# Performance work log

Hardware: AMD Instinct MI355X
Metric: run time of the kernel (lower is better)

Reference implementation:

```python
import jax, jax.numpy as jnp
import numpy as np

B, S, NU, ML, H, V = 32, 256, 4, 9, 768, 30522


def setup_inputs() -> dict:
    key = jax.random.key(0)
    ks = jax.random.split(key, 13)
    s = 1.0 / np.sqrt(H)
    return {
        "x": jax.random.randint(ks[0], (B, S), 0, V),
        "decoder_input": jax.random.normal(ks[1], (B, NU, H), jnp.float32) * 0.02,
        "encoder_output": jax.random.normal(ks[2], (B, S, H), jnp.float32) * 0.02,
        "hidden": jax.random.normal(ks[3], (1, B, H), jnp.float32) * 0.02,
        "max_len": ML,
        "teacher": jax.random.randint(ks[4], (B, NU, ML), 0, V),
        "embed_w": jax.random.normal(ks[5], (V, H), jnp.float32) * 0.02,
        "gru_w_ih": jax.random.uniform(ks[6], (3 * H, H), jnp.float32, -s, s),
        "gru_w_hh": jax.random.uniform(ks[7], (3 * H, H), jnp.float32, -s, s),
        "gru_b_ih": jax.random.uniform(ks[8], (3 * H,), jnp.float32, -s, s),
        "gru_b_hh": jax.random.uniform(ks[9], (3 * H,), jnp.float32, -s, s),
        "w_gen_w": jax.random.uniform(ks[10], (1, 3 * H), jnp.float32, -s, s),
        "w_gen_b": jax.random.uniform(ks[11], (1,), jnp.float32, -s, s),
    }


def reference(x, decoder_input, encoder_output, hidden, max_len, teacher,
              embed_w, gru_w_ih, gru_w_hh, gru_b_ih, gru_b_hh, w_gen_w, w_gen_b):
    pad_mask = (x == 0)                       # [B, S]
    b, nu, h_dim = decoder_input.shape
    h0 = hidden[0]                            # [B, H]

    # Teacher-forced input sequence for every (update, step): [NU*ML, B, H]
    tf = embed_w[teacher[:, :, :max_len - 1]]           # [B, NU, ML-1, H]
    tf = jnp.moveaxis(tf, 0, 2)                          # [NU, ML-1, B, H]
    first = jnp.swapaxes(decoder_input, 0, 1)[:, None]   # [NU, 1, B, H]
    ws = jnp.concatenate([first, tf], axis=1).reshape(nu * max_len, b, h_dim)

    def gru_cell(w, h):
        gi = w @ gru_w_ih.T + gru_b_ih        # [B, 3H]
        gh = h @ gru_w_hh.T + gru_b_hh
        i_r, i_z, i_n = jnp.split(gi, 3, axis=-1)
        h_r, h_z, h_n = jnp.split(gh, 3, axis=-1)
        r = jax.nn.sigmoid(i_r + h_r)
        z = jax.nn.sigmoid(i_z + h_z)
        n = jnp.tanh(i_n + r * h_n)
        return (1.0 - z) * n + z * h

    batch_idx = jnp.arange(b)[:, None]

    def step(h, w):
        h = gru_cell(w, h)                                    # [B, H]
        attn_e = jnp.einsum('bsh,bh->bs', encoder_output, h)  # [B, S]
        attn_e = jnp.where(pad_mask, -1e9, attn_e)
        attn_history = jax.nn.softmax(attn_e, axis=-1)        # [B, S]
        attn_vocab = jax.nn.softmax(h @ embed_w.T, axis=-1)   # [B, V]
        context = jnp.einsum('bs,bsh->bh', attn_history, encoder_output)
        gate_in = jnp.concatenate([w, h, context], axis=-1)   # [B, 3H]
        p_gen = jax.nn.sigmoid(gate_in @ w_gen_w.T + w_gen_b) # [B, 1]
        p_ctx = jnp.zeros_like(attn_vocab).at[batch_idx, x].add(attn_history)
        p_final = p_gen * attn_vocab + (1.0 - p_gen) * p_ctx  # [B, V]
        return h, p_final

    _, outs = jax.lax.scan(step, h0, ws)          # [NU*ML, B, V]
    outs = outs.reshape(nu, max_len, b, -1)       # [NU, ML, B, V]
    return jnp.transpose(outs, (2, 0, 1, 3))      # [B, NU, ML, V]
```

## Files before the change

kernel.cpp:

```cpp
#include <hip/hip_runtime.h>
#include <math.h>

#define BB_ 32
#define SS_ 256
#define HH_ 768
#define VV_ 30522
#define TT_ 36
#define MM_ 1152
#define NBLK_GRU 48

#define CE0 5860224
#define CE1 7433088
#define CE2 7875456
#define CE3 8317824
#define CE4 8323968

typedef __bf16 bf16x8 __attribute__((ext_vector_type(8)));
typedef __bf16 bf16x4 __attribute__((ext_vector_type(4)));
typedef float f32x4 __attribute__((ext_vector_type(4)));
typedef float f32x2 __attribute__((ext_vector_type(2)));
typedef unsigned int u32x4 __attribute__((ext_vector_type(4)));

__device__ __forceinline__ float sigmoidf_(float x) { return 1.f / (1.f + expf(-x)); }

__device__ __forceinline__ void async_load16(const void* g, void* l) {
  __builtin_amdgcn_global_load_lds(
      (const __attribute__((address_space(1))) void*)g,
      (__attribute__((address_space(3))) void*)l, 16, 0, 0);
}

__global__ __launch_bounds__(256) void cvt_all(const float* __restrict__ s0,
                                               const float* __restrict__ s1,
                                               const float* __restrict__ s2,
                                               const float* __restrict__ s3,
                                               const float* __restrict__ s4,
                                               __bf16* __restrict__ d0,
                                               __bf16* __restrict__ d1,
                                               __bf16* __restrict__ d2,
                                               __bf16* __restrict__ d3,
                                               __bf16* __restrict__ d4) {
  int i = blockIdx.x * 256 + threadIdx.x;
  const float* s; __bf16* d; int off;
  if (i < CE0)      { s = s0; d = d0; off = 0; }
  else if (i < CE1) { s = s1; d = d1; off = CE0; }
  else if (i < CE2) { s = s2; d = d2; off = CE1; }
  else if (i < CE3) { s = s3; d = d3; off = CE2; }
  else if (i < CE4) { s = s4; d = d4; off = CE3; }
  else return;
  int j = i - off;
  float4 v = reinterpret_cast<const float4*>(s)[j];
  bf16x4 o;
  o[0] = (__bf16)v.x; o[1] = (__bf16)v.y; o[2] = (__bf16)v.z; o[3] = (__bf16)v.w;
  reinterpret_cast<bf16x4*>(d)[j] = o;
}

__global__ __launch_bounds__(256) void build_ws(const float* __restrict__ dec,
                                                const int* __restrict__ teacher,
                                                const float* __restrict__ embed,
                                                __bf16* __restrict__ wsbf) {
  int idx = blockIdx.x * 256 + threadIdx.x;
  if (idx >= MM_ * HH_) return;
  int m = idx / HH_, k = idx - m * HH_;
  int tau = m >> 5, b = m & 31;
  int u = tau / 9, tt = tau - u * 9;
  float v;
  if (tt == 0) v = dec[((size_t)b * 4 + u) * HH_ + k];
  else v = embed[(size_t)teacher[(b * 4 + u) * 9 + tt - 1] * HH_ + k];
  wsbf[idx] = (__bf16)v;
}

__global__ __launch_bounds__(256) void enc_gate(const float* __restrict__ enc,
                                                const float* __restrict__ wgen,
                                                float* __restrict__ encg) {
  int row = blockIdx.x * 4 + (threadIdx.x >> 6);
  int lane = threadIdx.x & 63;
  const float* er = enc + (size_t)row * HH_;
  float ssum = 0.f;
#pragma unroll
  for (int i = 0; i < 12; ++i) ssum += er[i * 64 + lane] * wgen[1536 + i * 64 + lane];
  for (int off = 32; off; off >>= 1) ssum += __shfl_down(ssum, off);
  if (lane == 0) encg[row] = ssum;
}

template <int MODE>
__global__ __launch_bounds__(256) void gemm_bt2(const __bf16* __restrict__ A,
                                                const __bf16* __restrict__ Bm,
                                                float* __restrict__ C,
                                                float* __restrict__ rowsum,
                                                int Nreal, int ldC) {
  __shared__ __bf16 As[128 * 32];
  __shared__ __bf16 Bs[128 * 32];
  const int tid = threadIdx.x;
  const int lane = tid & 63, wave = tid >> 6;
  const int wm = wave >> 1, wn = wave & 1;
  const int q = lane >> 4, ln = lane & 15;
  const int m0 = blockIdx.y * 128, n0 = blockIdx.x * 128;
  const int srow = (wave << 5) + (lane >> 2);
  const int kc = lane & 3;
  const size_t aoff = (size_t)(m0 + srow) * HH_ + kc * 8;
  const size_t aoff2 = aoff + 16 * HH_;
  int br1 = n0 + srow;      if (br1 >= Nreal) br1 = Nreal - 1;
  int br2 = n0 + srow + 16; if (br2 >= Nreal) br2 = Nreal - 1;
  __bf16* lA1 = &As[srow * 32 + kc * 8];
  __bf16* lA2 = &As[(srow + 16) * 32 + kc * 8];
  __bf16* lB1 = &Bs[srow * 32 + kc * 8];
  __bf16* lB2 = &Bs[(srow + 16) * 32 + kc * 8];
  f32x4 acc[4][4] = {};
  for (int kb = 0; kb < 24; ++kb) {
    const int k0 = kb << 5;
    async_load16(A + aoff + k0, lA1);
    async_load16(A + aoff2 + k0, lA2);
    async_load16(Bm + (size_t)br1 * HH_ + kc * 8 + k0, lB1);
    async_load16(Bm + (size_t)br2 * HH_ + kc * 8 + k0, lB2);
    __syncthreads();
    bf16x8 af[4], bfr[4];
#pragma unroll
    for (int mi = 0; mi < 4; ++mi)
      af[mi] = *reinterpret_cast<const bf16x8*>(&As[(wm * 64 + mi * 16 + ln) * 32 + q * 8]);
#pragma unroll
    for (int ni = 0; ni < 4; ++ni)
      bfr[ni] = *reinterpret_cast<const bf16x8*>(&Bs[(wn * 64 + ni * 16 + ln) * 32 + q * 8]);
#pragma unroll
    for (int mi = 0; mi < 4; ++mi)
#pragma unroll
      for (int ni = 0; ni < 4; ++ni)
        acc[mi][ni] = __builtin_amdgcn_mfma_f32_16x16x32_bf16(af[mi], bfr[ni], acc[mi][ni], 0, 0, 0);
    __syncthreads();
  }
#pragma unroll
  for (int mi = 0; mi < 4; ++mi)
#pragma unroll
    for (int r2 = 0; r2 < 4; ++r2) {
      const int m = m0 + wm * 64 + mi * 16 + q * 4 + r2;
      if (MODE == 0) {
#pragma unroll
        for (int ni = 0; ni < 4; ++ni) {
          int n = n0 + wn * 64 + ni * 16 + ln;
          if (n < Nreal) C[(size_t)m * ldC + n] = acc[mi][ni][r2];
        }
      } else {
        float part = 0.f;
#pragma unroll
        for (int ni = 0; ni < 4; ++ni) {
          int n = n0 + wn * 64 + ni * 16 + ln;
          float e = expf(fminf(acc[mi][ni][r2], 60.f));
          if (n < Nreal) {
            __builtin_nontemporal_store(e, &C[(size_t)m * ldC + n]);
            part += e;
          }
        }
#pragma unroll
        for (int o = 1; o < 16; o <<= 1) part += __shfl_xor(part, o);
        if (ln == 0) atomicAdd(rowsum + m, part);
      }
    }
}

__global__ __launch_bounds__(128, 1) void gru_scan(const __bf16* __restrict__ hid_bf,
                                                   const float* __restrict__ H0,
                                                   const __bf16* __restrict__ Whh,
                                                   const float* __restrict__ GI,
                                                   const float* __restrict__ bih,
                                                   const float* __restrict__ bhh,
                                                   __bf16* __restrict__ Ah,
                                                   __bf16* __restrict__ Hx,
                                                   unsigned* __restrict__ flags) {
  __shared__ __bf16 WhhS[48 * HH_];
  const int tid = threadIdx.x, lane = tid & 63;
  const int mi = tid >> 6;
  const int q = lane >> 4, ln = lane & 15;
  const int jH = blockIdx.x * 16 + ln;
  for (int i = tid; i < 48 * 96; i += 128) {
    int row = i / 96, cs = i - row * 96;
    int g = row >> 4, jl = row & 15;
    bf16x8 v = *reinterpret_cast<const bf16x8*>(
        &Whh[((size_t)(g * 768 + blockIdx.x * 16 + jl)) * HH_ + cs * 8]);
    *reinterpret_cast<bf16x8*>(&WhhS[row * HH_ + ((cs ^ (row & 7)) * 8)]) = v;
  }
  const float bir = bih[jH], biz = bih[jH + 768], bin_ = bih[jH + 1536];
  const float bhr = bhh[jH], bhz = bhh[jH + 768], bhn = bhh[jH + 1536];
  float hc[4];
#pragma unroll
  for (int r2 = 0; r2 < 4; ++r2)
    hc[r2] = H0[(size_t)(mi * 16 + q * 4 + r2) * HH_ + jH];
  const __bf16* w0 = &WhhS[(0 + ln) * HH_];
  const __bf16* w1 = &WhhS[(16 + ln) * HH_];
  const __bf16* w2 = &WhhS[(32 + ln) * HH_];
  const int swz = (ln & 7) * 8;
  float gir[4], giz[4], gin[4];
#pragma unroll
  for (int r2 = 0; r2 < 4; ++r2) {
    const float* gi = GI + (size_t)(mi * 16 + q * 4 + r2) * 2304;
    gir[r2] = gi[jH]; giz[r2] = gi[jH + 768]; gin[r2] = gi[jH + 1536];
  }
  __syncthreads();
  for (int tau = 0; tau < TT_; ++tau) {
    const __bf16* arow = tau ? (Hx + (size_t)(((tau - 1) & 1) * 32 + mi * 16 + ln) * HH_)
                             : (hid_bf + (size_t)(mi * 16 + ln) * HH_);
    u32x4 raw[24];
#pragma unroll
    for (int kb = 0; kb < 24; ++kb) {
      const __bf16* ap = arow + kb * 32 + q * 8;
      asm volatile("global_load_dwordx4 %0, %1, off sc1"
                   : "=v"(raw[kb]) : "v"(ap) : "memory");
    }
    asm volatile("s_waitcnt vmcnt(0)" ::: "memory");
    __builtin_amdgcn_sched_barrier(0);
    f32x4 a0 = {}, a1 = {}, a2 = {};
#pragma unroll
    for (int kb = 0; kb < 24; ++kb) {
      bf16x8 a = __builtin_bit_cast(bf16x8, raw[kb]);
      int kl = (kb * 32 + q * 8) ^ swz;
      bf16x8 b0 = *reinterpret_cast<const bf16x8*>(w0 + kl);
      bf16x8 b1 = *reinterpret_cast<const bf16x8*>(w1 + kl);
      bf16x8 b2 = *reinterpret_cast<const bf16x8*>(w2 + kl);
      a0 = __builtin_amdgcn_mfma_f32_16x16x32_bf16(a, b0, a0, 0, 0, 0);
      a1 = __builtin_amdgcn_mfma_f32_16x16x32_bf16(a, b1, a1, 0, 0, 0);
      a2 = __builtin_amdgcn_mfma_f32_16x16x32_bf16(a, b2, a2, 0, 0, 0);
    }
    __bf16* hxc = Hx + (size_t)((tau & 1) * 32) * HH_;
#pragma unroll
    for (int r2 = 0; r2 < 4; ++r2) {
      int b = mi * 16 + q * 4 + r2;
      float r = sigmoidf_(gir[r2] + bir + a0[r2] + bhr);
      float z = sigmoidf_(giz[r2] + biz + a1[r2] + bhz);
      float n = tanhf(gin[r2] + bin_ + r * (a2[r2] + bhn));
      float h = (1.f - z) * n + z * hc[r2];
      hc[r2] = h;
      float hp = __shfl_xor(h, 1);
      __bf16 hb = (__bf16)h, hpb = (__bf16)hp;
      unsigned lo = (unsigned)__builtin_bit_cast(unsigned short, hb);
      unsigned hi = (unsigned)__builtin_bit_cast(unsigned short, hpb);
      if (!(ln & 1)) {
        unsigned u = lo | (hi << 16);
        *reinterpret_cast<unsigned*>(&Ah[((size_t)b * TT_ + tau) * HH_ + jH]) = u;
        if (tau < TT_ - 1)
          __hip_atomic_store(reinterpret_cast<unsigned*>(&hxc[(size_t)b * HH_ + jH]), u,
                             __ATOMIC_RELAXED, __HIP_MEMORY_SCOPE_AGENT);
      }
    }
    if (tau < TT_ - 1) {
      asm volatile("s_waitcnt vmcnt(0)" ::: "memory");
      if (lane == 0)
        __hip_atomic_store(&flags[(size_t)(blockIdx.x * 2 + mi) * 16], (unsigned)(tau + 1),
                           __ATOMIC_RELAXED, __HIP_MEMORY_SCOPE_AGENT);
      {
        const float* GIt = GI + (size_t)(tau + 1) * BB_ * 2304;
#pragma unroll
        for (int r2 = 0; r2 < 4; ++r2) {
          const float* gi = GIt + (size_t)(mi * 16 + q * 4 + r2) * 2304;
          gir[r2] = gi[jH]; giz[r2] = gi[jH + 768]; gin[r2] = gi[jH + 1536];
        }
      }
      const unsigned tgt = (unsigned)(tau + 1);
      int ok = 0, spin = 0;
      while (!ok) {
        unsigned v = (lane < NBLK_GRU)
            ? __hip_atomic_load(&flags[(size_t)(lane * 2 + mi) * 16], __ATOMIC_RELAXED,
                                __HIP_MEMORY_SCOPE_AGENT)
            : tgt;
        ok = __all((int)(v >= tgt));
        if (!ok) {
          __builtin_amdgcn_s_sleep(1);
          if (++spin > (1 << 20)) break;
        }
      }
    }
  }
}

__global__ __launch_bounds__(256) void attn_gemm(const __bf16* __restrict__ Ah,
                                                 const __bf16* __restrict__ encb,
                                                 float* __restrict__ E) {
  int b = blockIdx.x >> 2, stile = blockIdx.x & 3;
  int wave = threadIdx.x >> 6, lane = threadIdx.x & 63;
  int q = lane >> 4, ln = lane & 15;
  int s = stile * 64 + wave * 16 + ln;
  const __bf16* brow = encb + ((size_t)b * SS_ + s) * HH_;
  const __bf16* arow[3];
#pragma unroll
  for (int mt = 0; mt < 3; ++mt) {
    int tau = mt * 16 + ln; if (tau > 35) tau = 35;
    arow[mt] = Ah + ((size_t)b * TT_ + tau) * HH_;
  }
  f32x4 acc[3] = {};
#pragma unroll 4
  for (int kb = 0; kb < 24; ++kb) {
    int k0 = kb * 32 + q * 8;
    bf16x8 bb = *reinterpret_cast<const bf16x8*>(brow + k0);
#pragma unroll
    for (int mt = 0; mt < 3; ++mt) {
      bf16x8 aa = *reinterpret_cast<const bf16x8*>(arow[mt] + k0);
      acc[mt] = __builtin_amdgcn_mfma_f32_16x16x32_bf16(aa, bb, acc[mt], 0, 0, 0);
    }
  }
#pragma unroll
  for (int mt = 0; mt < 3; ++mt)
#pragma unroll
    for (int r2 = 0; r2 < 4; ++r2) {
      int tau = mt * 16 + q * 4 + r2;
      if (tau < 36) E[((size_t)b * TT_ + tau) * SS_ + s] = acc[mt][r2];
    }
}

__global__ __launch_bounds__(256) void softmax_pg(const float* __restrict__ E,
                                                  const int* __restrict__ x,
                                                  const float* __restrict__ encg,
                                                  const __bf16* __restrict__ wsbf,
                                                  const __bf16* __restrict__ Ah,
                                                  const float* __restrict__ wgen,
                                                  const float* __restrict__ wgenb,
                                                  float* __restrict__ attn,
                                                  float* __restrict__ pg) {
  int m = blockIdx.x;
  int b = m / TT_, tau = m - b * TT_;
  int m_in = tau * 32 + b;
  int t = threadIdx.x;
  __shared__ float red[256];
  __shared__ float r1[256], r2[256], r3[256];
  float e = E[(size_t)m * SS_ + t];
  if (x[b * SS_ + t] == 0) e = -1000000000.0f;
  red[t] = e; __syncthreads();
  for (int off = 128; off; off >>= 1) {
    if (t < off) red[t] = fmaxf(red[t], red[t + off]);
    __syncthreads();
  }
  float mx = red[0];
  float p = expf(e - mx);
  float dsum = 0.f;
#pragma unroll
  for (int i = 0; i < 3; ++i) {
    int k = t + i * 256;
    dsum += (float)wsbf[(size_t)m_in * HH_ + k] * wgen[k];
    dsum += (float)Ah[(size_t)m * HH_ + k] * wgen[768 + k];
  }
  float pe = p * encg[b * SS_ + t];
  r1[t] = p; r2[t] = pe; r3[t] = dsum; __syncthreads();
  for (int off = 128; off; off >>= 1) {
    if (t < off) { r1[t] += r1[t + off]; r2[t] += r2[t + off]; r3[t] += r3[t + off]; }
    __syncthreads();
  }
  float Z = r1[0];
  attn[(size_t)m * SS_ + t] = p / Z;
  if (t == 0) pg[m] = sigmoidf_(r3[0] + r2[0] / Z + wgenb[0]);
}

__global__ __launch_bounds__(256) void finalize(float* __restrict__ C,
                                                const float* __restrict__ rowsum,
                                                const float* __restrict__ pg) {
  int m = blockIdx.y;
  float scale = pg[m] / rowsum[m];
  f32x2* row = reinterpret_cast<f32x2*>(C + (size_t)m * VV_);
#pragma unroll
  for (int j = 0; j < 8; ++j) {
    int i2 = blockIdx.x * 2048 + j * 256 + threadIdx.x;
    if (i2 < VV_ / 2) {
      f32x2 v = __builtin_nontemporal_load(&row[i2]);
      v[0] *= scale; v[1] *= scale;
      __builtin_nontemporal_store(v, &row[i2]);
    }
  }
}

__global__ __launch_bounds__(256) void scatter_ctx(float* __restrict__ C,
                                                   const float* __restrict__ attn,
                                                   const float* __restrict__ pg,
                                                   const int* __restrict__ x) {
  int m = blockIdx.x, s = threadIdx.x;
  int b = m / TT_;
  float v = (1.f - pg[m]) * attn[(size_t)m * SS_ + s];
  int col = x[b * SS_ + s];
  atomicAdd(C + (size_t)m * VV_ + col, v);
}

extern "C" void kernel_launch(void* const* d_in, const int* in_sizes, int n_in,
                              void* d_out, int out_size, void* d_ws, size_t ws_size,
                              hipStream_t stream) {
  const int*   x       = (const int*)d_in[0];
  const float* dec     = (const float*)d_in[1];
  const float* enc     = (const float*)d_in[2];
  const float* hidden  = (const float*)d_in[3];
  const int*   teacher = (const int*)d_in[5];
  const float* embed   = (const float*)d_in[6];
  const float* wih     = (const float*)d_in[7];
  const float* whh     = (const float*)d_in[8];
  const float* bih     = (const float*)d_in[9];
  const float* bhh     = (const float*)d_in[10];
  const float* wgen    = (const float*)d_in[11];
  const float* wgenb   = (const float*)d_in[12];
  float* out = (float*)d_out;

  char* w = (char*)d_ws;
  __bf16* embed_bf = (__bf16*)w;  w += (size_t)VV_ * HH_ * 2;
  __bf16* enc_bf   = (__bf16*)w;  w += (size_t)BB_ * SS_ * HH_ * 2;
  __bf16* wih_bf   = (__bf16*)w;  w += (size_t)2304 * HH_ * 2;
  __bf16* whh_bf   = (__bf16*)w;  w += (size_t)2304 * HH_ * 2;
  __bf16* ws_bf    = (__bf16*)w;  w += (size_t)MM_ * HH_ * 2;
  __bf16* hid_bf   = (__bf16*)w;  w += (size_t)BB_ * HH_ * 2;
  __bf16* A_h      = (__bf16*)w;  w += (size_t)MM_ * HH_ * 2;
  float*  GI       = (float*)w;   w += (size_t)MM_ * 2304 * 4;
  float*  E        = (float*)w;   w += (size_t)MM_ * SS_ * 4;
  float*  attn     = (float*)w;   w += (size_t)MM_ * SS_ * 4;
  float*  encg     = (float*)w;   w += (size_t)BB_ * SS_ * 4;
  float*  pg       = (float*)w;   w += 8192;
  char*   ctl      = w;           w += 16384;
  __bf16* Hx       = (__bf16*)w;  w += (size_t)2 * BB_ * HH_ * 2;
  float*    rowsum = (float*)ctl;
  unsigned* flags  = (unsigned*)(ctl + 4864);

  hipMemsetAsync(ctl, 0, 16384, stream);

  cvt_all<<<(CE4 + 255) / 256, 256, 0, stream>>>(embed, enc, wih, whh, hidden,
                                                 embed_bf, enc_bf, wih_bf, whh_bf, hid_bf);

  build_ws<<<(MM_ * HH_ + 255) / 256, 256, 0, stream>>>(dec, teacher, embed, ws_bf);

  gemm_bt2<0><<<dim3(2304 / 128, MM_ / 128), 256, 0, stream>>>(ws_bf, wih_bf, GI, nullptr, 2304, 2304);

  enc_gate<<<BB_ * SS_ / 4, 256, 0, stream>>>(enc, wgen, encg);

  gru_scan<<<NBLK_GRU, 128, 0, stream>>>(hid_bf, hidden, whh_bf, GI, bih, bhh, A_h, Hx, flags);

  attn_gemm<<<BB_ * 4, 256, 0, stream>>>(A_h, enc_bf, E);
  softmax_pg<<<MM_, 256, 0, stream>>>(E, x, encg, ws_bf, A_h, wgen, wgenb, attn, pg);

  gemm_bt2<1><<<dim3((VV_ + 127) / 128, MM_ / 128), 256, 0, stream>>>(A_h, embed_bf, out, rowsum, VV_, VV_);

  finalize<<<dim3(8, MM_), 256, 0, stream>>>(out, rowsum, pg);
  scatter_ctx<<<MM_, 256, 0, stream>>>(out, attn, pg, x);
}
```

Measured before the change: 775.0 us.

## Recompute vocab GEMM twice to fuse softmax normalization and drop finalize pass

Splits the vocab projection into two passes. The first pass only computes exp row sums. The second pass recomputes the GEMM and writes the normalized, p_gen-scaled probabilities directly. This removes the separate finalize kernel, which read and rewrote the whole 1152x30522 fp32 output. In exchange the ~54 GFLOP bf16 GEMM runs twice, trading extra compute for one fewer full pass over the output in memory.

```diff
diff --git a/kernel.cpp b/kernel.cpp
--- a/kernel.cpp
+++ b/kernel.cpp
@@ -18,7 +18,6 @@
 typedef __bf16 bf16x8 __attribute__((ext_vector_type(8)));
 typedef __bf16 bf16x4 __attribute__((ext_vector_type(4)));
 typedef float f32x4 __attribute__((ext_vector_type(4)));
-typedef float f32x2 __attribute__((ext_vector_type(2)));
 typedef unsigned int u32x4 __attribute__((ext_vector_type(4)));
 
 __device__ __forceinline__ float sigmoidf_(float x) { return 1.f / (1.f + expf(-x)); }
@@ -87,6 +86,7 @@
                                                 const __bf16* __restrict__ Bm,
                                                 float* __restrict__ C,
                                                 float* __restrict__ rowsum,
+                                                const float* __restrict__ pg,
                                                 int Nreal, int ldC) {
   __shared__ __bf16 As[128 * 32];
   __shared__ __bf16 Bs[128 * 32];
@@ -138,20 +138,26 @@
           int n = n0 + wn * 64 + ni * 16 + ln;
           if (n < Nreal) C[(size_t)m * ldC + n] = acc[mi][ni][r2];
         }
-      } else {
+      } else if (MODE == 1) {
         float part = 0.f;
 #pragma unroll
         for (int ni = 0; ni < 4; ++ni) {
           int n = n0 + wn * 64 + ni * 16 + ln;
           float e = expf(fminf(acc[mi][ni][r2], 60.f));
-          if (n < Nreal) {
-            __builtin_nontemporal_store(e, &C[(size_t)m * ldC + n]);
-            part += e;
-          }
+          if (n < Nreal) part += e;
         }
 #pragma unroll
         for (int o = 1; o < 16; o <<= 1) part += __shfl_xor(part, o);
         if (ln == 0) atomicAdd(rowsum + m, part);
+      } else {
+        const float scale = pg[m] / rowsum[m];
+#pragma unroll
+        for (int ni = 0; ni < 4; ++ni) {
+          int n = n0 + wn * 64 + ni * 16 + ln;
+          float e = expf(fminf(acc[mi][ni][r2], 60.f));
+          if (n < Nreal)
+            __builtin_nontemporal_store(e * scale, &C[(size_t)m * ldC + n]);
+        }
       }
     }
 }
@@ -345,23 +351,6 @@
   if (t == 0) pg[m] = sigmoidf_(r3[0] + r2[0] / Z + wgenb[0]);
 }
 
-__global__ __launch_bounds__(256) void finalize(float* __restrict__ C,
-                                                const float* __restrict__ rowsum,
-                                                const float* __restrict__ pg) {
-  int m = blockIdx.y;
-  float scale = pg[m] / rowsum[m];
-  f32x2* row = reinterpret_cast<f32x2*>(C + (size_t)m * VV_);
-#pragma unroll
-  for (int j = 0; j < 8; ++j) {
-    int i2 = blockIdx.x * 2048 + j * 256 + threadIdx.x;
-    if (i2 < VV_ / 2) {
-      f32x2 v = __builtin_nontemporal_load(&row[i2]);
-      v[0] *= scale; v[1] *= scale;
-      __builtin_nontemporal_store(v, &row[i2]);
-    }
-  }
-}
-
 __global__ __launch_bounds__(256) void scatter_ctx(float* __restrict__ C,
                                                    const float* __restrict__ attn,
                                                    const float* __restrict__ pg,
@@ -415,17 +404,18 @@
 
   build_ws<<<(MM_ * HH_ + 255) / 256, 256, 0, stream>>>(dec, teacher, embed, ws_bf);
 
-  gemm_bt2<0><<<dim3(2304 / 128, MM_ / 128), 256, 0, stream>>>(ws_bf, wih_bf, GI, nullptr, 2304, 2304);
+  gemm_bt2<0><<<dim3(2304 / 128, MM_ / 128), 256, 0, stream>>>(ws_bf, wih_bf, GI, nullptr, nullptr, 2304, 2304);
 
   enc_gate<<<BB_ * SS_ / 4, 256, 0, stream>>>(enc, wgen, encg);
 
   gru_scan<<<NBLK_GRU, 128, 0, stream>>>(hid_bf, hidden, whh_bf, GI, bih, bhh, A_h, Hx, flags);
+
+  gemm_bt2<1><<<dim3((VV_ + 127) / 128, MM_ / 128), 256, 0, stream>>>(A_h, embed_bf, nullptr, rowsum, nullptr, VV_, VV_);
 
   attn_gemm<<<BB_ * 4, 256, 0, stream>>>(A_h, enc_bf, E);
   softmax_pg<<<MM_, 256, 0, stream>>>(E, x, encg, ws_bf, A_h, wgen, wgenb, attn, pg);
 
-  gemm_bt2<1><<<dim3((VV_ + 127) / 128, MM_ / 128), 256, 0, stream>>>(A_h, embed_bf, out, rowsum, VV_, VV_);
-
-  finalize<<<dim3(8, MM_), 256, 0, stream>>>(out, rowsum, pg);
+  gemm_bt2<2><<<dim3((VV_ + 127) / 128, MM_ / 128), 256, 0, stream>>>(A_h, embed_bf, out, rowsum, pg, VV_, VV_);
+
   scatter_ctx<<<MM_, 256, 0, stream>>>(out, attn, pg, x);
 }
```

After: 857.6 us. +10.7%, slower.
